# Kernel optimization log

Hardware: AMD Instinct MI355X
Metric: run time of the kernel (lower is better)

Reference implementation:

```python
import jax, jax.numpy as jnp
import numpy as np

B, N, M, K, C, OUT = 4, 16384, 4096, 16, 128, 256
MAX_RADIUS = 0.3
LN_EPS = 1e-5
STABLE_EPS = 1e-6
BIG = 1e9


def _xavier(key, shape):
    lim = np.sqrt(6.0 / (shape[0] + shape[1])).astype(np.float32)
    return jax.random.uniform(key, shape, jnp.float32, -lim, lim)


def _layer_norm(x, w, b):
    mu = x.mean(axis=-1, keepdims=True)
    var = ((x - mu) ** 2).mean(axis=-1, keepdims=True)
    return (x - mu) / jnp.sqrt(var + LN_EPS) * w + b


def setup_inputs() -> dict:
    key = jax.random.key(0)
    ks = jax.random.split(key, 8)
    points = jax.random.uniform(ks[0], (B, N, 3), jnp.float32)   # unit cube -> radius 0.3 is meaningful
    feats = jax.random.normal(ks[1], (B, N, C), jnp.float32)
    center_idx = jax.random.randint(ks[2], (B, M), 0, N)
    return {
        "points": points,
        "feats": feats,
        "center_idx": center_idx,
        "ln1_w": jnp.ones((2 * C,), jnp.float32),
        "ln1_b": jnp.zeros((2 * C,), jnp.float32),
        "W1": _xavier(ks[3], (2 * C, C)),
        "b1": jnp.zeros((C,), jnp.float32),
        "W2": _xavier(ks[4], (C, C)),
        "b2": jnp.zeros((C,), jnp.float32),
        "Wm": _xavier(ks[5], (C, OUT)),
        "bm": jnp.zeros((OUT,), jnp.float32),
        "ln2_w": jnp.ones((OUT,), jnp.float32),
        "ln2_b": jnp.zeros((OUT,), jnp.float32),
        "res_scale": jnp.float32(0.5),
    }


def reference(points, feats, center_idx, ln1_w, ln1_b, W1, b1, W2, b2, Wm, bm, ln2_w, ln2_b, res_scale):
    b_, n_, _ = points.shape
    m_ = center_idx.shape[1]
    c_ = feats.shape[-1]
    k_ = min(K, n_)

    # gather center coordinates: (B,M,3)
    centers = jnp.take_along_axis(points, jnp.broadcast_to(center_idx[:, :, None], (b_, m_, 3)), axis=1)

    # stable squared pairwise distances (B,M,N)
    a_sq = (centers ** 2).sum(-1, keepdims=True)            # (B,M,1)
    b_sq = (points ** 2).sum(-1)[:, None, :]                # (B,1,N)
    dist2 = a_sq + b_sq - 2.0 * jnp.einsum('bmd,bnd->bmn', centers, points)
    dist2 = jnp.clip(dist2, 0.0, None)
    dist = jnp.sqrt(dist2 + STABLE_EPS)

    # radius mask then k smallest distances
    masked = jnp.where(dist <= MAX_RADIUS, dist, BIG)
    _, idx = jax.lax.top_k(-masked, k_)                     # ascending distances
    knn_idx = jnp.clip(idx, 0, n_ - 1)                      # (B,M,K)

    # gather neighbor features (B,M,K,C)
    neigh = jnp.take_along_axis(
        feats, knn_idx.reshape(b_, m_ * k_)[:, :, None], axis=1
    ).reshape(b_, m_, k_, c_)

    # gather center features (B,M,C)
    cf = jnp.take_along_axis(feats, jnp.broadcast_to(center_idx[:, :, None], (b_, m_, c_)), axis=1)

    # channel attention MLP over concat(center, neighbor) -> sigmoid weights
    combo = jnp.concatenate([jnp.broadcast_to(cf[:, :, None, :], (b_, m_, k_, c_)), neigh], axis=-1)
    cn = _layer_norm(combo, ln1_w, ln1_b)
    h = jax.nn.relu(cn @ W1 + b1)
    w = jax.nn.sigmoid(h @ W2 + b2)                         # (B,M,K,C)

    weighted = (neigh * w).mean(axis=2)                     # (B,M,C)
    fused = cf + res_scale * weighted
    out = jax.nn.relu(fused @ Wm + bm)                      # (B,M,OUT)
    out = _layer_norm(out, ln2_w, ln2_b)
    return out, knn_idx
```

## Files before the change

### kernel.cpp

```cpp
#include <hip/hip_runtime.h>
#include <hip/hip_bf16.h>
#include <math.h>

#define B_ 4
#define N_ 16384
#define M_ 4096
#define K_ 16
#define C_ 128
#define OUT_ 256
#define S_CHUNKS 16
#define CHUNK 1024
#define TPB 256
#define MAX_R 0.3f
#define BIGF 1e9f
#define LN_EPS_F 1e-5f
#define SEPS 1e-6f
#define BM (B_ * M_)


typedef __attribute__((ext_vector_type(8))) short bf16x8;
typedef __attribute__((ext_vector_type(4))) float f32x4;

__device__ __forceinline__ unsigned short bfu(float f) {
  __hip_bfloat16 h = __float2bfloat16(f);
  return *reinterpret_cast<unsigned short*>(&h);
}
__device__ __forceinline__ float b2f(unsigned short u) {
  unsigned x = ((unsigned)u) << 16;
  return __uint_as_float(x);
}
__device__ __forceinline__ float fast_sigmoid(float x) {
  return __builtin_amdgcn_rcpf(1.0f + __expf(-x));
}

__global__ __launch_bounds__(TPB) void knn_partial_kernel(
    const float* __restrict__ points, const int* __restrict__ cidx,
    float* __restrict__ pvals, int* __restrict__ pidx)
{
#pragma clang fp contract(off)
  const int s  = blockIdx.x;
  const int mg = blockIdx.y;
  const int b  = blockIdx.z;
  const int tid = threadIdx.x;

  __shared__ float4 pts[CHUNK];
  __shared__ unsigned long long buf[12][TPB];

  const int j0 = s * CHUNK;
  for (int e = tid; e < CHUNK; e += TPB) {
    int j = j0 + e;
    float x = points[(b * N_ + j) * 3 + 0];
    float y = points[(b * N_ + j) * 3 + 1];
    float z = points[(b * N_ + j) * 3 + 2];
    float bq = (x * x + z * z) + y * y;
    pts[e] = make_float4(x, y, z, bq);
  }

  const int m  = mg * TPB + tid;
  const int cm = b * M_ + m;
  const int ci = cidx[cm];
  const float cx = points[(b * N_ + ci) * 3 + 0];
  const float cy = points[(b * N_ + ci) * 3 + 1];
  const float cz = points[(b * N_ + ci) * 3 + 2];
  const float aq = (cx * cx + cz * cz) + cy * cy;
  __syncthreads();

  float v[16];
  int   id[16];
#pragma unroll
  for (int t = 0; t < 16; t++) { v[t] = 3.4e38f; id[t] = 0; }
  float v15q = 0.0905f;
  int cnt = 0;

  for (int e0 = 0; e0 < CHUNK; e0 += 4) {
#pragma unroll
    for (int u = 0; u < 4; u++) {
      int e = e0 + u;
      float4 p = pts[e];
      float dot = fmaf(cz, p.z, fmaf(cy, p.y, cx * p.x));
      float d2 = fmaf(-2.0f, dot, aq + p.w);
      if (d2 < v15q) {
        buf[cnt][tid] =
            ((unsigned long long)__float_as_uint(d2) << 32) | (unsigned)(j0 + e);
        cnt++;
      }
    }
    if (__any(cnt >= 8)) {
      for (int ss = 0; ss < 12; ss++) {
        if (ss < cnt) {
          unsigned long long kk = buf[ss][tid];
          float d2v = __uint_as_float((unsigned)(kk >> 32));
          int j = (int)(kk & 0xffffffffULL);
          float d2c = fmaxf(d2v, 0.0f);
          float dist = __fsqrt_rn(d2c + SEPS);
          float md = (dist <= MAX_R) ? dist : BIGF;
          if (md < v[15]) {
            bool cg[16];
#pragma unroll
            for (int t = 0; t < 16; t++) cg[t] = (v[t] > md);
#pragma unroll
            for (int t = 15; t >= 1; t--) {
              v[t]  = cg[t - 1] ? v[t - 1]  : (cg[t] ? md : v[t]);
              id[t] = cg[t - 1] ? id[t - 1] : (cg[t] ? j  : id[t]);
            }
            if (cg[0]) { v[0] = md; id[0] = j; }
          }
        }
      }
      cnt = 0;
      float v15 = v[15];
      v15q = fminf(0.0905f, fmaf(v15, v15, 1e-6f));
    }
  }

  for (int ss = 0; ss < 12; ss++) {
    if (ss < cnt) {
      unsigned long long kk = buf[ss][tid];
      float d2v = __uint_as_float((unsigned)(kk >> 32));
      int j = (int)(kk & 0xffffffffULL);
      float d2c = fmaxf(d2v, 0.0f);
      float dist = __fsqrt_rn(d2c + SEPS);
      float md = (dist <= MAX_R) ? dist : BIGF;
      if (md < v[15]) {
        bool cg[16];
#pragma unroll
        for (int t = 0; t < 16; t++) cg[t] = (v[t] > md);
#pragma unroll
        for (int t = 15; t >= 1; t--) {
          v[t]  = cg[t - 1] ? v[t - 1]  : (cg[t] ? md : v[t]);
          id[t] = cg[t - 1] ? id[t - 1] : (cg[t] ? j  : id[t]);
        }
        if (cg[0]) { v[0] = md; id[0] = j; }
      }
    }
  }

#pragma unroll
  for (int t = 0; t < 16; t++) {
    int o = (s * 16 + t) * BM + cm;
    pvals[o] = v[t];
    pidx[o]  = id[t];
  }
}

__global__ __launch_bounds__(64) void knn_merge_kernel(
    const float* __restrict__ pvals, const int* __restrict__ pidx,
    int* __restrict__ kidx, float* __restrict__ dout)
{
  const int cm = blockIdx.x * 64 + threadIdx.x;

  unsigned long long key[16];
#pragma unroll
  for (int t = 0; t < 16; t++) {
    int o = t * BM + cm;
    unsigned int vb = __float_as_uint(pvals[o]);
    key[t] = ((unsigned long long)vb << 32) | (unsigned int)pidx[o];
  }
  for (int s = 1; s < S_CHUNKS; s++) {
    for (int t2 = 0; t2 < 16; t2++) {
      int o = (s * 16 + t2) * BM + cm;
      unsigned int vb = __float_as_uint(pvals[o]);
      unsigned long long Kk = ((unsigned long long)vb << 32) | (unsigned int)pidx[o];
      if (Kk >= key[15]) break;
      bool cg[16];
#pragma unroll
      for (int t = 0; t < 16; t++) cg[t] = (key[t] > Kk);
#pragma unroll
      for (int t = 15; t >= 1; t--)
        key[t] = cg[t - 1] ? key[t - 1] : (cg[t] ? Kk : key[t]);
      if (cg[0]) key[0] = Kk;
    }
  }
#pragma unroll
  for (int t = 0; t < 16; t++) {
    int j = (int)(key[t] & 0xffffffffULL);
    kidx[cm * K_ + t] = j;
    dout[(size_t)BM * OUT_ + (size_t)cm * K_ + t] = (float)j;
  }
}

__global__ __launch_bounds__(TPB) void convert_weights_kernel(
    const float* __restrict__ W1, const float* __restrict__ W2,
    const float* __restrict__ Wm,
    unsigned short* __restrict__ Wt1, unsigned short* __restrict__ Wt2,
    unsigned short* __restrict__ Wtm)
{
  int t = blockIdx.x * TPB + threadIdx.x;
  if (t < 128 * 256) {
    int col = t >> 8, k = t & 255;
    Wt1[t] = bfu(W1[k * 128 + col]);
  } else if (t < 128 * 256 + 128 * 128) {
    int u = t - 128 * 256;
    int col = u >> 7, k = u & 127;
    Wt2[u] = bfu(W2[k * 128 + col]);
  } else {
    int w = t - (128 * 256 + 128 * 128);
    int col = w >> 7, k = w & 127;
    Wtm[w] = bfu(Wm[k * 256 + col]);
  }
}

__global__ __launch_bounds__(TPB, 5) void fuse_mlp_kernel(
    const float* __restrict__ feats, const int* __restrict__ cidx,
    const int* __restrict__ kidx,
    const float* __restrict__ ln1w, const float* __restrict__ ln1b,
    const unsigned short* __restrict__ Wt1, const float* __restrict__ b1,
    const unsigned short* __restrict__ Wt2, const float* __restrict__ b2,
    const unsigned short* __restrict__ Wtm, const float* __restrict__ bm,
    const float* __restrict__ ln2w, const float* __restrict__ ln2b,
    const float* __restrict__ res_scale,
    float* __restrict__ dout)
{
  const int cm0 = blockIdx.x * 2;
  const int b   = cm0 >> 12;
  const int tid = threadIdx.x;
  const int lane = tid & 63, wv = tid >> 6;

  __shared__ float cf[2][C_];
  __shared__ __align__(16) unsigned short nb[2][K_][136];
  __shared__ __align__(16) char pool[2 * K_ * 272 * 2];
  __shared__ __align__(16) unsigned short fvb[2][136];
  __shared__ float outb[2][OUT_];
  __shared__ float red[4];
  __shared__ int nidx[2][K_];

  typedef unsigned short cn_t[K_][272];
  typedef unsigned short hw_t[K_][136];
  cn_t* cn  = (cn_t*)pool;
  hw_t* hb  = (hw_t*)pool;
  hw_t* wbb = (hw_t*)(pool + 2 * K_ * 136 * 2);

  if (tid < 32) {
    int c = tid >> 4, t = tid & 15;
    nidx[c][t] = kidx[(cm0 + c) * K_ + t];
  }
  __syncthreads();

  {
    for (int t = tid; t < 1088; t += TPB) {
      int c = (t >= 544) ? 1 : 0;
      int u = t - c * 544;
      int row = u >> 5, c4 = u & 31;
      int src = (row == 0) ? cidx[cm0 + c] : nidx[c][row - 1];
      float4 val = *(const float4*)&feats[((size_t)b * N_ + src) * C_ + c4 * 4];
      if (row == 0) {
        *(float4*)&cf[c][c4 * 4] = val;
      } else {
        int r = row - 1, cc = c4 * 4;
        nb[c][r][cc]     = bfu(val.x);
        nb[c][r][cc + 1] = bfu(val.y);
        nb[c][r][cc + 2] = bfu(val.z);
        nb[c][r][cc + 3] = bfu(val.w);
      }
    }
  }
  __syncthreads();

  for (int kk = 0; kk < 4; kk++) {
    int k = wv * 4 + kk;
#pragma unroll
    for (int c = 0; c < 2; c++) {
      float x0 = cf[c][lane];
      float x1 = cf[c][lane + 64];
      float x2 = b2f(nb[c][k][lane]);
      float x3 = b2f(nb[c][k][lane + 64]);
      float ssum = ((x0 + x1) + (x2 + x3));
#pragma unroll
      for (int off = 1; off < 64; off <<= 1) ssum += __shfl_xor(ssum, off, 64);
      float mu = ssum * (1.0f / 256.0f);
      float d0 = x0 - mu, d1 = x1 - mu, d2 = x2 - mu, d3 = x3 - mu;
      float vs = fmaf(d0, d0, fmaf(d1, d1, fmaf(d2, d2, d3 * d3)));
#pragma unroll
      for (int off = 1; off < 64; off <<= 1) vs += __shfl_xor(vs, off, 64);
      float var = vs * (1.0f / 256.0f);
      float rs = __builtin_amdgcn_rsqf(var + LN_EPS_F);
      cn[c][k][lane]       = bfu(fmaf(d0 * rs, ln1w[lane],       ln1b[lane]));
      cn[c][k][lane + 64]  = bfu(fmaf(d1 * rs, ln1w[lane + 64],  ln1b[lane + 64]));
      cn[c][k][lane + 128] = bfu(fmaf(d2 * rs, ln1w[lane + 128], ln1b[lane + 128]));
      cn[c][k][lane + 192] = bfu(fmaf(d3 * rs, ln1w[lane + 192], ln1b[lane + 192]));
    }
  }
  __syncthreads();

  const int r16 = lane & 15;
  const int kg  = lane >> 4;
  const int c0 = (2 * wv) * 16 + r16;
  const int c1 = (2 * wv + 1) * 16 + r16;

  f32x4 a0[2] = {{0.f,0.f,0.f,0.f},{0.f,0.f,0.f,0.f}};
  f32x4 a1[2] = {{0.f,0.f,0.f,0.f},{0.f,0.f,0.f,0.f}};
#pragma unroll
  for (int kt = 0; kt < 8; kt++) {
    int k0 = kt * 32 + kg * 8;
    bf16x8 g0 = *(const bf16x8*)&Wt1[(size_t)c0 * 256 + k0];
    bf16x8 g1 = *(const bf16x8*)&Wt1[(size_t)c1 * 256 + k0];
#pragma unroll
    for (int c = 0; c < 2; c++) {
      bf16x8 af = *(const bf16x8*)&cn[c][r16][k0];
      a0[c] = __builtin_amdgcn_mfma_f32_16x16x32_bf16(af, g0, a0[c], 0, 0, 0);
      a1[c] = __builtin_amdgcn_mfma_f32_16x16x32_bf16(af, g1, a1[c], 0, 0, 0);
    }
  }
  __syncthreads();
#pragma unroll
  for (int c = 0; c < 2; c++)
#pragma unroll
    for (int r = 0; r < 4; r++) {
      int ro = kg * 4 + r;
      hb[c][ro][c0] = bfu(fmaxf(a0[c][r] + b1[c0], 0.f));
      hb[c][ro][c1] = bfu(fmaxf(a1[c][r] + b1[c1], 0.f));
    }
  __syncthreads();

  f32x4 s0[2] = {{0.f,0.f,0.f,0.f},{0.f,0.f,0.f,0.f}};
  f32x4 s1[2] = {{0.f,0.f,0.f,0.f},{0.f,0.f,0.f,0.f}};
#pragma unroll
  for (int kt = 0; kt < 4; kt++) {
    int k0 = kt * 32 + kg * 8;
    bf16x8 g0 = *(const bf16x8*)&Wt2[(size_t)c0 * 128 + k0];
    bf16x8 g1 = *(const bf16x8*)&Wt2[(size_t)c1 * 128 + k0];
#pragma unroll
    for (int c = 0; c < 2; c++) {
      bf16x8 af = *(const bf16x8*)&hb[c][r16][k0];
      s0[c] = __builtin_amdgcn_mfma_f32_16x16x32_bf16(af, g0, s0[c], 0, 0, 0);
      s1[c] = __builtin_amdgcn_mfma_f32_16x16x32_bf16(af, g1, s1[c], 0, 0, 0);
    }
  }
#pragma unroll
  for (int c = 0; c < 2; c++)
#pragma unroll
    for (int r = 0; r < 4; r++) {
      int ro = kg * 4 + r;
      wbb[c][ro][c0] = bfu(fast_sigmoid(s0[c][r] + b2[c0]));
      wbb[c][ro][c1] = bfu(fast_sigmoid(s1[c][r] + b2[c1]));
    }
  __syncthreads();

  {
    int c = tid >> 7, col = tid & 127;
    float ssum = 0.f;
#pragma unroll
    for (int kq = 0; kq < 16; kq++)
      ssum = fmaf(b2f(nb[c][kq][col]), b2f(wbb[c][kq][col]), ssum);
    float wmean = ssum * (1.0f / 16.0f);
    fvb[c][col] = bfu(fmaf(res_scale[0], wmean, cf[c][col]));
  }
  __syncthreads();

#pragma unroll
  for (int i = 0; i < 4; i++) {
    int cb = (wv * 4 + i) * 16;
    f32x4 acc[2] = {{0.f,0.f,0.f,0.f},{0.f,0.f,0.f,0.f}};
#pragma unroll
    for (int kt = 0; kt < 4; kt++) {
      int k0 = kt * 32 + kg * 8;
      bf16x8 gf = *(const bf16x8*)&Wtm[(size_t)(cb + r16) * 128 + k0];
#pragma unroll
      for (int c = 0; c < 2; c++) {
        bf16x8 af = *(const bf16x8*)&fvb[c][k0];
        acc[c] = __builtin_amdgcn_mfma_f32_16x16x32_bf16(af, gf, acc[c], 0, 0, 0);
      }
    }
    if (kg == 0) {
      int cc = cb + r16;
#pragma unroll
      for (int c = 0; c < 2; c++)
        outb[c][cc] = fmaxf(acc[c][0] + bm[cc], 0.f);
    }
  }
  __syncthreads();

  for (int c = 0; c < 2; c++) {
    float outx = outb[c][tid];
    float s = outx;
#pragma unroll
    for (int off = 1; off < 64; off <<= 1) s += __shfl_xor(s, off, 64);
    if (lane == 0) red[wv] = s;
    __syncthreads();
    float mu = (red[0] + red[1] + red[2] + red[3]) * (1.0f / 256.0f);
    float d = outx - mu;
    float s2 = d * d;
#pragma unroll
    for (int off = 1; off < 64; off <<= 1) s2 += __shfl_xor(s2, off, 64);
    __syncthreads();
    if (lane == 0) red[wv] = s2;
    __syncthreads();
    float var = (red[0] + red[1] + red[2] + red[3]) * (1.0f / 256.0f);
    float rs2 = __builtin_amdgcn_rsqf(var + LN_EPS_F);
    dout[(size_t)(cm0 + c) * OUT_ + tid] = fmaf(d * rs2, ln2w[tid], ln2b[tid]);
    __syncthreads();
  }
}

extern "C" void kernel_launch(void* const* d_in, const int* in_sizes, int n_in,
                              void* d_out, int out_size, void* d_ws, size_t ws_size,
                              hipStream_t stream) {
  const float* points = (const float*)d_in[0];
  const float* feats  = (const float*)d_in[1];
  const int*   cidx   = (const int*)  d_in[2];
  const float* ln1w   = (const float*)d_in[3];
  const float* ln1b   = (const float*)d_in[4];
  const float* W1     = (const float*)d_in[5];
  const float* b1     = (const float*)d_in[6];
  const float* W2     = (const float*)d_in[7];
  const float* b2     = (const float*)d_in[8];
  const float* Wm     = (const float*)d_in[9];
  const float* bm     = (const float*)d_in[10];
  const float* ln2w   = (const float*)d_in[11];
  const float* ln2b   = (const float*)d_in[12];
  const float* rscale = (const float*)d_in[13];

  float* out = (float*)d_out;
  char*  ws  = (char*)d_ws;
  float* pvals = (float*)ws;
  int*   pidx  = (int*)(ws + 16777216);
  int*   kidx  = (int*)(ws + 33554432);
  unsigned short* Wt1 = (unsigned short*)(ws + 34603008);
  unsigned short* Wt2 = (unsigned short*)(ws + 34603008 + 65536);
  unsigned short* Wtm = (unsigned short*)(ws + 34603008 + 65536 + 32768);

  convert_weights_kernel<<<(128 * 256 + 128 * 128 + 256 * 128 + TPB - 1) / TPB,
                           TPB, 0, stream>>>(W1, W2, Wm, Wt1, Wt2, Wtm);
  knn_partial_kernel<<<dim3(S_CHUNKS, M_ / TPB, B_), TPB, 0, stream>>>(points, cidx, pvals, pidx);
  knn_merge_kernel<<<BM / 64, 64, 0, stream>>>(pvals, pidx, kidx, out);
  fuse_mlp_kernel<<<BM / 2, TPB, 0, stream>>>(feats, cidx, kidx,
                                              ln1w, ln1b, Wt1, b1, Wt2, b2, Wtm, bm,
                                              ln2w, ln2b, rscale, out);
}
```

Baseline: 411.0 us.

## Process four centers per 512-thread block in fused MLP kernel

The fused attention-MLP kernel now handles four center points per block with 512 threads instead of two with 256. Each wave computes one 16-column slice of the W1/W2 outputs across four centers, so every global weight fragment feeds four MFMAs instead of two. This cuts weight-load traffic per center and halves the block count. In exchange, each block uses about twice the shared memory and the launch bound drops to 2 blocks, which lowers occupancy and latency hiding for the feature gathers.

```diff
diff --git a/kernel.cpp b/kernel.cpp
--- a/kernel.cpp
+++ b/kernel.cpp
@@ -200,7 +200,7 @@
   }
 }
 
-__global__ __launch_bounds__(TPB, 5) void fuse_mlp_kernel(
+__global__ __launch_bounds__(512, 2) void fuse_mlp_kernel(
     const float* __restrict__ feats, const int* __restrict__ cidx,
     const int* __restrict__ kidx,
     const float* __restrict__ ln1w, const float* __restrict__ ln1b,
@@ -211,55 +211,53 @@
     const float* __restrict__ res_scale,
     float* __restrict__ dout)
 {
-  const int cm0 = blockIdx.x * 2;
+  const int cm0 = blockIdx.x * 4;
   const int b   = cm0 >> 12;
   const int tid = threadIdx.x;
   const int lane = tid & 63, wv = tid >> 6;
 
-  __shared__ float cf[2][C_];
-  __shared__ __align__(16) unsigned short nb[2][K_][136];
-  __shared__ __align__(16) char pool[2 * K_ * 272 * 2];
-  __shared__ __align__(16) unsigned short fvb[2][136];
-  __shared__ float outb[2][OUT_];
-  __shared__ float red[4];
-  __shared__ int nidx[2][K_];
+  __shared__ float cf[4][C_];
+  __shared__ __align__(16) unsigned short nb[4][K_][136];
+  __shared__ __align__(16) char pool[4 * K_ * 272 * 2];
+  __shared__ __align__(16) unsigned short fvb[4][136];
+  __shared__ float outb[4][OUT_];
+  __shared__ float red[2][4];
+  __shared__ int nidx[4][K_];
 
   typedef unsigned short cn_t[K_][272];
   typedef unsigned short hw_t[K_][136];
   cn_t* cn  = (cn_t*)pool;
   hw_t* hb  = (hw_t*)pool;
-  hw_t* wbb = (hw_t*)(pool + 2 * K_ * 136 * 2);
-
-  if (tid < 32) {
+  hw_t* wbb = (hw_t*)(pool + 4 * K_ * 136 * 2);
+
+  if (tid < 64) {
     int c = tid >> 4, t = tid & 15;
     nidx[c][t] = kidx[(cm0 + c) * K_ + t];
   }
   __syncthreads();
 
-  {
-    for (int t = tid; t < 1088; t += TPB) {
-      int c = (t >= 544) ? 1 : 0;
-      int u = t - c * 544;
-      int row = u >> 5, c4 = u & 31;
-      int src = (row == 0) ? cidx[cm0 + c] : nidx[c][row - 1];
-      float4 val = *(const float4*)&feats[((size_t)b * N_ + src) * C_ + c4 * 4];
-      if (row == 0) {
-        *(float4*)&cf[c][c4 * 4] = val;
-      } else {
-        int r = row - 1, cc = c4 * 4;
-        nb[c][r][cc]     = bfu(val.x);
-        nb[c][r][cc + 1] = bfu(val.y);
-        nb[c][r][cc + 2] = bfu(val.z);
-        nb[c][r][cc + 3] = bfu(val.w);
-      }
-    }
-  }
-  __syncthreads();
-
-  for (int kk = 0; kk < 4; kk++) {
-    int k = wv * 4 + kk;
-#pragma unroll
-    for (int c = 0; c < 2; c++) {
+  for (int t = tid; t < 2176; t += 512) {
+    int c = t / 544;
+    int u = t - c * 544;
+    int row = u >> 5, c4 = u & 31;
+    int src = (row == 0) ? cidx[cm0 + c] : nidx[c][row - 1];
+    float4 val = *(const float4*)&feats[((size_t)b * N_ + src) * C_ + c4 * 4];
+    if (row == 0) {
+      *(float4*)&cf[c][c4 * 4] = val;
+    } else {
+      int r = row - 1, cc = c4 * 4;
+      nb[c][r][cc]     = bfu(val.x);
+      nb[c][r][cc + 1] = bfu(val.y);
+      nb[c][r][cc + 2] = bfu(val.z);
+      nb[c][r][cc + 3] = bfu(val.w);
+    }
+  }
+  __syncthreads();
+
+  for (int kk = 0; kk < 2; kk++) {
+    int k = wv * 2 + kk;
+#pragma unroll
+    for (int c = 0; c < 4; c++) {
       float x0 = cf[c][lane];
       float x1 = cf[c][lane + 64];
       float x2 = b2f(nb[c][k][lane]);
@@ -284,55 +282,46 @@
 
   const int r16 = lane & 15;
   const int kg  = lane >> 4;
-  const int c0 = (2 * wv) * 16 + r16;
-  const int c1 = (2 * wv + 1) * 16 + r16;
-
-  f32x4 a0[2] = {{0.f,0.f,0.f,0.f},{0.f,0.f,0.f,0.f}};
-  f32x4 a1[2] = {{0.f,0.f,0.f,0.f},{0.f,0.f,0.f,0.f}};
+  const int col1 = wv * 16 + r16;
+
+  f32x4 a[4] = {{0.f,0.f,0.f,0.f},{0.f,0.f,0.f,0.f},{0.f,0.f,0.f,0.f},{0.f,0.f,0.f,0.f}};
 #pragma unroll
   for (int kt = 0; kt < 8; kt++) {
     int k0 = kt * 32 + kg * 8;
-    bf16x8 g0 = *(const bf16x8*)&Wt1[(size_t)c0 * 256 + k0];
-    bf16x8 g1 = *(const bf16x8*)&Wt1[(size_t)c1 * 256 + k0];
-#pragma unroll
-    for (int c = 0; c < 2; c++) {
+    bf16x8 g = *(const bf16x8*)&Wt1[(size_t)col1 * 256 + k0];
+#pragma unroll
+    for (int c = 0; c < 4; c++) {
       bf16x8 af = *(const bf16x8*)&cn[c][r16][k0];
-      a0[c] = __builtin_amdgcn_mfma_f32_16x16x32_bf16(af, g0, a0[c], 0, 0, 0);
-      a1[c] = __builtin_amdgcn_mfma_f32_16x16x32_bf16(af, g1, a1[c], 0, 0, 0);
-    }
-  }
-  __syncthreads();
-#pragma unroll
-  for (int c = 0; c < 2; c++)
+      a[c] = __builtin_amdgcn_mfma_f32_16x16x32_bf16(af, g, a[c], 0, 0, 0);
+    }
+  }
+  __syncthreads();
+#pragma unroll
+  for (int c = 0; c < 4; c++)
 #pragma unroll
     for (int r = 0; r < 4; r++) {
       int ro = kg * 4 + r;
-      hb[c][ro][c0] = bfu(fmaxf(a0[c][r] + b1[c0], 0.f));
-      hb[c][ro][c1] = bfu(fmaxf(a1[c][r] + b1[c1], 0.f));
-    }
-  __syncthreads();
-
-  f32x4 s0[2] = {{0.f,0.f,0.f,0.f},{0.f,0.f,0.f,0.f}};
-  f32x4 s1[2] = {{0.f,0.f,0.f,0.f},{0.f,0.f,0.f,0.f}};
+      hb[c][ro][col1] = bfu(fmaxf(a[c][r] + b1[col1], 0.f));
+    }
+  __syncthreads();
+
+  f32x4 s[4] = {{0.f,0.f,0.f,0.f},{0.f,0.f,0.f,0.f},{0.f,0.f,0.f,0.f},{0.f,0.f,0.f,0.f}};
 #pragma unroll
   for (int kt = 0; kt < 4; kt++) {
     int k0 = kt * 32 + kg * 8;
-    bf16x8 g0 = *(const bf16x8*)&Wt2[(size_t)c0 * 128 + k0];
-    bf16x8 g1 = *(const bf16x8*)&Wt2[(size_t)c1 * 128 + k0];
-#pragma unroll
-    for (int c = 0; c < 2; c++) {
+    bf16x8 g = *(const bf16x8*)&Wt2[(size_t)col1 * 128 + k0];
+#pragma unroll
+    for (int c = 0; c < 4; c++) {
       bf16x8 af = *(const bf16x8*)&hb[c][r16][k0];
-      s0[c] = __builtin_amdgcn_mfma_f32_16x16x32_bf16(af, g0, s0[c], 0, 0, 0);
-      s1[c] = __builtin_amdgcn_mfma_f32_16x16x32_bf16(af, g1, s1[c], 0, 0, 0);
-    }
-  }
-#pragma unroll
-  for (int c = 0; c < 2; c++)
+      s[c] = __builtin_amdgcn_mfma_f32_16x16x32_bf16(af, g, s[c], 0, 0, 0);
+    }
+  }
+#pragma unroll
+  for (int c = 0; c < 4; c++)
 #pragma unroll
     for (int r = 0; r < 4; r++) {
       int ro = kg * 4 + r;
-      wbb[c][ro][c0] = bfu(fast_sigmoid(s0[c][r] + b2[c0]));
-      wbb[c][ro][c1] = bfu(fast_sigmoid(s1[c][r] + b2[c1]));
+      wbb[c][ro][col1] = bfu(fast_sigmoid(s[c][r] + b2[col1]));
     }
   __syncthreads();
 
@@ -348,15 +337,15 @@
   __syncthreads();
 
 #pragma unroll
-  for (int i = 0; i < 4; i++) {
-    int cb = (wv * 4 + i) * 16;
-    f32x4 acc[2] = {{0.f,0.f,0.f,0.f},{0.f,0.f,0.f,0.f}};
+  for (int i = 0; i < 2; i++) {
+    int cb = (wv * 2 + i) * 16;
+    f32x4 acc[4] = {{0.f,0.f,0.f,0.f},{0.f,0.f,0.f,0.f},{0.f,0.f,0.f,0.f},{0.f,0.f,0.f,0.f}};
 #pragma unroll
     for (int kt = 0; kt < 4; kt++) {
       int k0 = kt * 32 + kg * 8;
       bf16x8 gf = *(const bf16x8*)&Wtm[(size_t)(cb + r16) * 128 + k0];
 #pragma unroll
-      for (int c = 0; c < 2; c++) {
+      for (int c = 0; c < 4; c++) {
         bf16x8 af = *(const bf16x8*)&fvb[c][k0];
         acc[c] = __builtin_amdgcn_mfma_f32_16x16x32_bf16(af, gf, acc[c], 0, 0, 0);
       }
@@ -364,31 +353,37 @@
     if (kg == 0) {
       int cc = cb + r16;
 #pragma unroll
-      for (int c = 0; c < 2; c++)
+      for (int c = 0; c < 4; c++)
         outb[c][cc] = fmaxf(acc[c][0] + bm[cc], 0.f);
     }
   }
   __syncthreads();
 
-  for (int c = 0; c < 2; c++) {
-    float outx = outb[c][tid];
-    float s = outx;
-#pragma unroll
-    for (int off = 1; off < 64; off <<= 1) s += __shfl_xor(s, off, 64);
-    if (lane == 0) red[wv] = s;
-    __syncthreads();
-    float mu = (red[0] + red[1] + red[2] + red[3]) * (1.0f / 256.0f);
-    float d = outx - mu;
-    float s2 = d * d;
-#pragma unroll
-    for (int off = 1; off < 64; off <<= 1) s2 += __shfl_xor(s2, off, 64);
-    __syncthreads();
-    if (lane == 0) red[wv] = s2;
-    __syncthreads();
-    float var = (red[0] + red[1] + red[2] + red[3]) * (1.0f / 256.0f);
-    float rs2 = __builtin_amdgcn_rsqf(var + LN_EPS_F);
-    dout[(size_t)(cm0 + c) * OUT_ + tid] = fmaf(d * rs2, ln2w[tid], ln2b[tid]);
-    __syncthreads();
+  {
+    int grp = tid >> 8;
+    int col = tid & 255;
+    int wvin = (tid >> 6) & 3;
+    for (int cpass = 0; cpass < 2; cpass++) {
+      int c = cpass * 2 + grp;
+      float outx = outb[c][col];
+      float su = outx;
+#pragma unroll
+      for (int off = 1; off < 64; off <<= 1) su += __shfl_xor(su, off, 64);
+      if (lane == 0) red[grp][wvin] = su;
+      __syncthreads();
+      float mu = (red[grp][0] + red[grp][1] + red[grp][2] + red[grp][3]) * (1.0f / 256.0f);
+      float d = outx - mu;
+      float s2 = d * d;
+#pragma unroll
+      for (int off = 1; off < 64; off <<= 1) s2 += __shfl_xor(s2, off, 64);
+      __syncthreads();
+      if (lane == 0) red[grp][wvin] = s2;
+      __syncthreads();
+      float var = (red[grp][0] + red[grp][1] + red[grp][2] + red[grp][3]) * (1.0f / 256.0f);
+      float rs2 = __builtin_amdgcn_rsqf(var + LN_EPS_F);
+      dout[(size_t)(cm0 + c) * OUT_ + col] = fmaf(d * rs2, ln2w[col], ln2b[col]);
+      __syncthreads();
+    }
   }
 }
 
@@ -423,7 +418,7 @@
                            TPB, 0, stream>>>(W1, W2, Wm, Wt1, Wt2, Wtm);
   knn_partial_kernel<<<dim3(S_CHUNKS, M_ / TPB, B_), TPB, 0, stream>>>(points, cidx, pvals, pidx);
   knn_merge_kernel<<<BM / 64, 64, 0, stream>>>(pvals, pidx, kidx, out);
-  fuse_mlp_kernel<<<BM / 2, TPB, 0, stream>>>(feats, cidx, kidx,
+  fuse_mlp_kernel<<<BM / 4, 512, 0, stream>>>(feats, cidx, kidx,
                                               ln1w, ln1b, Wt1, b1, Wt2, b2, Wtm, bm,
                                               ln2w, ln2b, rscale, out);
 }
```

Result: faster. 372.1 us (-9.5%).
